# Optimization experiments

Hardware: AMD Instinct MI355X
Metric: run time of the kernel (lower is better)

Reference implementation:

```python
import jax, jax.numpy as jnp
import numpy as np

EMBED_DIM = 1024

def setup_inputs() -> dict:
    key = jax.random.key(0)
    kx, kwq, kbq, kwk, kbk, kwv, kbv = jax.random.split(key, 7)
    d = EMBED_DIM
    s = 1.0 / np.sqrt(d)
    x = jax.random.normal(kx, (4, 2048, d), dtype=jnp.float32)
    # nn.Linear weights are [out, in]; we store transposed [in, out] for x @ W
    Wq = jax.random.uniform(kwq, (d, d), jnp.float32, -s, s)
    bq = jax.random.uniform(kbq, (d,), jnp.float32, -s, s)
    Wk = jax.random.uniform(kwk, (d, d), jnp.float32, -s, s)
    bk = jax.random.uniform(kbk, (d,), jnp.float32, -s, s)
    Wv = jax.random.uniform(kwv, (d, d), jnp.float32, -s, s)
    bv = jax.random.uniform(kbv, (d,), jnp.float32, -s, s)
    return {"x": x, "Wq": Wq, "bq": bq, "Wk": Wk, "bk": bk, "Wv": Wv, "bv": bv}

def reference(x, Wq, bq, Wk, bk, Wv, bv):
    d = x.shape[-1]
    q = x @ Wq + bq            # [B, S, D]
    k = x @ Wk + bk            # [B, S, D]
    v = x @ Wv + bv            # [B, S, D]
    scores = jnp.einsum('bsd,btd->bst', q, k) / jnp.sqrt(jnp.asarray(d, x.dtype))
    attn = jax.nn.softmax(scores, axis=-1)  # [B, S, S]
    return jnp.einsum('bst,btd->bsd', attn, v)
```

## Files before the change

kernel.cpp:

```cpp
#include <hip/hip_runtime.h>
#include <hip/hip_bf16.h>
#include <stdint.h>


typedef short bf16x8 __attribute__((ext_vector_type(8)));
typedef float f32x4 __attribute__((ext_vector_type(4)));
typedef unsigned short us4 __attribute__((ext_vector_type(4)));
typedef unsigned short us8 __attribute__((ext_vector_type(8)));
typedef _Float16 h8v __attribute__((ext_vector_type(8)));
typedef unsigned short us;

#define B_ 4
#define S_ 2048
#define D_ 1024

__device__ __forceinline__ us f2bf(float f) {
  unsigned int u = __float_as_uint(f);
  unsigned int r = (u + 0x7fffu + ((u >> 16) & 1u)) >> 16;
  return (us)r;
}

__device__ __forceinline__ void gl2lds16(void* lds, const void* g) {
  __builtin_amdgcn_global_load_lds(
      (const __attribute__((address_space(1))) unsigned int*)(uintptr_t)g,
      (__attribute__((address_space(3))) unsigned int*)(uintptr_t)lds,
      16, 0, 0);
}

__device__ __forceinline__ void sched_fence() { __builtin_amdgcn_sched_barrier(0); }
__device__ __forceinline__ void barrier_f() {
  sched_fence(); __builtin_amdgcn_s_barrier(); sched_fence();
}

template<int BM, int R0, int R1>
__device__ __forceinline__ void stageR(us* buf, const us* gA, size_t sA,
                                       const us* gB, size_t sB,
                                       int wave, int lane) {
  int slot = ((lane & 7) ^ (lane >> 3)) << 4;
  char* l = (char*)buf;
#pragma unroll
  for (int r = R0; r < R1; ++r) {
    int row = r * 64 + wave * 8 + (lane >> 3);
    const char* src;
    if (r * 64 < BM)
      src = (const char*)gA + (size_t)row * sA + slot;
    else
      src = (const char*)gB + (size_t)(row - BM) * sB + slot;
    gl2lds16(l + r * 8192 + wave * 1024, src);
  }
}

template<int EPI, int BM, int BN, int WNS>
__global__ __launch_bounds__(512, 2) void gemm8p(
    const us* __restrict__ Aall, const us* __restrict__ Ball,
    size_t aBatch, size_t bBatch, int sAe, int sBe, int nt,
    const float* __restrict__ bias1, void* __restrict__ outp,
    us* __restrict__ vtb) {
  __shared__ __align__(16) us lds[3][(BM + BN) * 64];
  int tid = threadIdx.x, lane = tid & 63, wave = tid >> 6;
  int wm = wave / WNS, wn = wave % WNS;
  int m0 = blockIdx.x * BM, n0 = blockIdx.y * BN;
  size_t bz = blockIdx.z;
  const us* gA = Aall + bz * aBatch + (size_t)m0 * sAe;
  const us* gB = Ball + bz * bBatch + (size_t)n0 * sBe;
  size_t sA = (size_t)sAe * 2, sB = (size_t)sBe * 2;

  stageR<BM, 0, 6>(lds[0], gA, sA, gB, sB, wave, lane);
  stageR<BM, 0, 6>(lds[1], gA + 64, sA, gB + 64, sB, wave, lane);

  int r15 = lane & 15, kg = lane >> 4, l7 = lane & 7;
  int x0 = (kg ^ l7) << 4;
  f32x4 acc[4][4] = {};

  for (int t = 0; t < nt; ++t) {
    if (t == nt - 1) asm volatile("s_waitcnt vmcnt(0)" ::: "memory");
    else             asm volatile("s_waitcnt vmcnt(6)" ::: "memory");
    barrier_f();
    const us* buf = lds[t % 3];
    us* nbuf = (us*)lds[(t + 2) % 3];
    bool dostage = (t + 2 < nt);
    const us* gA2 = gA + (size_t)(t + 2) * 64;
    const us* gB2 = gB + (size_t)(t + 2) * 64;
    const char* pa = (const char*)buf + (size_t)(wm * 64 + r15) * 128;
    const char* pb = (const char*)buf + (size_t)(BM + wn * 64 + r15) * 128;

    if (dostage) stageR<BM, 0, 3>(nbuf, gA2, sA, gB2, sB, wave, lane);
    bf16x8 A0[4], B0[4];
#pragma unroll
    for (int f = 0; f < 4; ++f) A0[f] = *(const bf16x8*)(pa + f * 2048 + x0);
#pragma unroll
    for (int f = 0; f < 4; ++f) B0[f] = *(const bf16x8*)(pb + f * 2048 + x0);
    __builtin_amdgcn_s_setprio(1);
#pragma unroll
    for (int fn = 0; fn < 4; ++fn)
#pragma unroll
      for (int fm = 0; fm < 4; ++fm)
        acc[fm][fn] = __builtin_amdgcn_mfma_f32_16x16x32_bf16(A0[fm], B0[fn], acc[fm][fn], 0, 0, 0);
    __builtin_amdgcn_s_setprio(0);

    if (dostage) stageR<BM, 3, 6>(nbuf, gA2, sA, gB2, sB, wave, lane);
    bf16x8 A1[4], B1[4];
#pragma unroll
    for (int f = 0; f < 4; ++f) A1[f] = *(const bf16x8*)(pa + f * 2048 + (x0 ^ 64));
#pragma unroll
    for (int f = 0; f < 4; ++f) B1[f] = *(const bf16x8*)(pb + f * 2048 + (x0 ^ 64));
    __builtin_amdgcn_s_setprio(1);
#pragma unroll
    for (int fn = 0; fn < 4; ++fn)
#pragma unroll
      for (int fm = 0; fm < 4; ++fm)
        acc[fm][fn] = __builtin_amdgcn_mfma_f32_16x16x32_bf16(A1[fm], B1[fn], acc[fm][fn], 0, 0, 0);
    __builtin_amdgcn_s_setprio(0);
  }

#pragma unroll
  for (int fm = 0; fm < 4; ++fm)
#pragma unroll
    for (int fn = 0; fn < 4; ++fn) {
      int col = n0 + wn * 64 + fn * 16 + r15;
      int row0 = m0 + wm * 64 + fm * 16 + ((lane >> 4) << 2);
      if constexpr (EPI == 3) {
        int mat = col >> 10;
        if (mat == 0) {
          us* ob = (us*)outp;
#pragma unroll
          for (int r = 0; r < 4; ++r)
            ob[(size_t)(row0 + r) * D_ + col] = f2bf(acc[fm][fn][r]);
        } else {
          float bb = bias1[col & 1023];
          int b = row0 >> 11, trow = row0 & 2047, dcol = col & 1023;
          us4 v4 = {f2bf(acc[fm][fn][0] + bb), f2bf(acc[fm][fn][1] + bb),
                    f2bf(acc[fm][fn][2] + bb), f2bf(acc[fm][fn][3] + bb)};
          *(us4*)(vtb + (size_t)b * D_ * S_ + (size_t)dcol * S_ + trow) = v4;
        }
      } else {
        float* ob = (float*)outp + bz * (size_t)(S_ * D_);
#pragma unroll
        for (int r = 0; r < 4; ++r)
          ob[(size_t)(row0 + r) * D_ + col] = acc[fm][fn][r];
      }
    }
}

__global__ __launch_bounds__(512, 2) void s2k(
    const us* __restrict__ Aall, const us* __restrict__ Ball,
    const float* __restrict__ cvp, _Float16* __restrict__ scores) {
  __shared__ __align__(16) us lds3[3][16384];
  const int tid = threadIdx.x, lane = tid & 63, wave = tid >> 6;
  const int wm = wave >> 2, wn = wave & 3;
  const int m0 = blockIdx.x * 256, n0 = blockIdx.y * 256;
  const size_t bz = blockIdx.z;
  const char* gA = (const char*)(Aall + bz * (size_t)(S_ * D_) + (size_t)m0 * D_);
  const char* gB = (const char*)(Ball + bz * (size_t)(S_ * D_) + (size_t)n0 * D_);
  const size_t sA = (size_t)D_ * 2, sB = (size_t)D_ * 2;
  const int nt = 32;

  const int r15 = lane & 15, kg = lane >> 4;
  const int srcslot = (((lane & 3) ^ ((lane >> 3) & 3)) << 4);
  const int srow = wave * 16 + (lane >> 2);

  auto stage = [&](int bi, int t) {
    char* l = (char*)lds3[bi];
    const size_t koff = (size_t)t * 64;
#pragma unroll
    for (int r = 0; r < 4; ++r) {
      int row = r * 128 + srow;
      const char* src = (row < 256)
          ? gA + (size_t)row * sA + koff + srcslot
          : gB + (size_t)(row - 256) * sB + koff + srcslot;
      gl2lds16(l + r * 8192 + wave * 1024, src);
    }
  };

  stage(0, 0);
  stage(1, 1);

  f32x4 acc[8][4] = {};
  for (int t = 0; t < nt; ++t) {
    if (t == nt - 1) asm volatile("s_waitcnt vmcnt(0)" ::: "memory");
    else             asm volatile("s_waitcnt vmcnt(4)" ::: "memory");
    barrier_f();
    if (t + 2 < nt) stage((t + 2) % 3, t + 2);
    const char* buf = (const char*)lds3[t % 3];

    bf16x8 Af[8], Bf[4];
#pragma unroll
    for (int f = 0; f < 8; ++f) {
      int tr = wm * 128 + f * 16 + r15;
      Af[f] = *(const bf16x8*)(buf + tr * 64 + ((kg ^ ((tr >> 1) & 3)) << 4));
    }
#pragma unroll
    for (int n = 0; n < 4; ++n) {
      int tr = 256 + wn * 64 + n * 16 + r15;
      Bf[n] = *(const bf16x8*)(buf + tr * 64 + ((kg ^ ((tr >> 1) & 3)) << 4));
    }
    __builtin_amdgcn_s_setprio(1);
#pragma unroll
    for (int n = 0; n < 4; ++n)
#pragma unroll
      for (int f = 0; f < 8; ++f)
        acc[f][n] = __builtin_amdgcn_mfma_f32_16x16x32_bf16(Af[f], Bf[n], acc[f][n], 0, 0, 0);
    __builtin_amdgcn_s_setprio(0);
  }

  _Float16* sc = scores + bz * (size_t)(S_ * S_);
  const float* cb = cvp + bz * (size_t)S_;
#pragma unroll
  for (int fm = 0; fm < 8; ++fm)
#pragma unroll
    for (int fn = 0; fn < 4; ++fn) {
      int col = n0 + wn * 64 + fn * 16 + r15;
      int row0 = m0 + wm * 128 + fm * 16 + ((lane >> 4) << 2);
      float cv = cb[col];
#pragma unroll
      for (int r = 0; r < 4; ++r)
        sc[(size_t)(row0 + r) * S_ + col] = (_Float16)((acc[fm][fn][r] + cv) * 0.03125f);
    }
}

__global__ __launch_bounds__(256) void mprep(const us* __restrict__ wkb,
                                             const us* __restrict__ wqb,
                                             us* __restrict__ mtb) {
  int tid = threadIdx.x, lane = tid & 63, wave = tid >> 6;
  int j0 = blockIdx.x * 64, i0 = blockIdx.y * 64;
  int r15 = lane & 15, kg = lane >> 4;
  f32x4 acc[4] = {};
  for (int kk = 0; kk < D_; kk += 32) {
    bf16x8 a = *(const bf16x8*)(wkb + (size_t)(j0 + wave * 16 + r15) * D_ + kk + kg * 8);
#pragma unroll
    for (int f = 0; f < 4; ++f) {
      bf16x8 b = *(const bf16x8*)(wqb + (size_t)(i0 + f * 16 + r15) * D_ + kk + kg * 8);
      acc[f] = __builtin_amdgcn_mfma_f32_16x16x32_bf16(a, b, acc[f], 0, 0, 0);
    }
  }
#pragma unroll
  for (int f = 0; f < 4; ++f)
#pragma unroll
    for (int r = 0; r < 4; ++r)
      mtb[(size_t)(j0 + wave * 16 + kg * 4 + r) * D_ + i0 + f * 16 + r15] = f2bf(acc[f][r]);
}

__global__ __launch_bounds__(256) void uprep(const float* __restrict__ Wk,
                                             const float* __restrict__ bq,
                                             float* __restrict__ u) {
  int lane = threadIdx.x & 63, wave = threadIdx.x >> 6;
  int i = blockIdx.x * 4 + wave;
  const float* row = Wk + (size_t)i * D_;
  float s = 0.f;
#pragma unroll
  for (int e = 0; e < 4; ++e) {
    float4 a = *(const float4*)(row + e * 256 + lane * 4);
    float4 b = *(const float4*)(bq + e * 256 + lane * 4);
    s += a.x * b.x + a.y * b.y + a.z * b.z + a.w * b.w;
  }
#pragma unroll
  for (int o = 32; o; o >>= 1) s += __shfl_xor(s, o);
  if (lane == 0) u[i] = s;
}

__global__ __launch_bounds__(256) void cvec(const float* __restrict__ x,
                                            const float* __restrict__ u,
                                            float* __restrict__ c) {
  int lane = threadIdx.x & 63, wave = threadIdx.x >> 6;
  int i = blockIdx.x * 4 + wave;
  const float* row = x + (size_t)i * D_;
  float s = 0.f;
#pragma unroll
  for (int e = 0; e < 4; ++e) {
    float4 a = *(const float4*)(row + e * 256 + lane * 4);
    float4 b = *(const float4*)(u + e * 256 + lane * 4);
    s += a.x * b.x + a.y * b.y + a.z * b.z + a.w * b.w;
  }
#pragma unroll
  for (int o = 32; o; o >>= 1) s += __shfl_xor(s, o);
  if (lane == 0) c[i] = s;
}

__global__ __launch_bounds__(256) void wcast(const float* __restrict__ Wq,
                                             const float* __restrict__ Wk,
                                             us* __restrict__ wqb,
                                             us* __restrict__ wkb) {
  size_t i = ((size_t)blockIdx.x * 256 + threadIdx.x) * 8;
  const float* src = blockIdx.y ? Wk : Wq;
  us* dst = blockIdx.y ? wkb : wqb;
  float4 f0 = *(const float4*)(src + i);
  float4 f1 = *(const float4*)(src + i + 4);
  float vals[8] = {f0.x, f0.y, f0.z, f0.w, f1.x, f1.y, f1.z, f1.w};
  union { bf16x8 v; us s_[8]; } H;
#pragma unroll
  for (int e = 0; e < 8; ++e) H.s_[e] = f2bf(vals[e]);
  *(bf16x8*)(dst + i) = H.v;
}

__global__ __launch_bounds__(256) void wtv(const float* __restrict__ W,
                                           us* __restrict__ o) {
  __shared__ us hs[64][65];
  int n0 = blockIdx.x * 64, k0 = blockIdx.y * 64;
  int tid = threadIdx.x;
#pragma unroll
  for (int i = 0; i < 16; ++i) {
    int idx = tid + i * 256;
    int r = idx >> 6, c = idx & 63;
    hs[r][c] = f2bf(W[(size_t)(k0 + r) * D_ + (n0 + c)]);
  }
  __syncthreads();
#pragma unroll
  for (int i = 0; i < 16; ++i) {
    int idx = tid + i * 256;
    int r = idx >> 6, c = idx & 63;
    o[(size_t)(n0 + r) * D_ + (k0 + c)] = hs[c][r];
  }
}

__global__ __launch_bounds__(256) void xcast(const float* __restrict__ x,
                                             us* __restrict__ xb) {
  size_t i = ((size_t)blockIdx.x * 256 + threadIdx.x) * 8;
  float4 f0 = *(const float4*)(x + i);
  float4 f1 = *(const float4*)(x + i + 4);
  float vals[8] = {f0.x, f0.y, f0.z, f0.w, f1.x, f1.y, f1.z, f1.w};
  union { bf16x8 v; us s_[8]; } H;
#pragma unroll
  for (int e = 0; e < 8; ++e) H.s_[e] = f2bf(vals[e]);
  *(bf16x8*)(xb + i) = H.v;
}

__global__ __launch_bounds__(256) void softmax_k(const _Float16* __restrict__ scores,
                                                 us* __restrict__ pb) {
  int row = blockIdx.x, tid = threadIdx.x, lane = tid & 63, wave = tid >> 6;
  const _Float16* s = scores + (size_t)row * S_;
  h8v a8 = *(const h8v*)(s + tid * 8);
  float a[8];
#pragma unroll
  for (int e = 0; e < 8; ++e) a[e] = (float)a8[e];
  float m = a[0];
#pragma unroll
  for (int e = 1; e < 8; ++e) m = fmaxf(m, a[e]);
#pragma unroll
  for (int o = 32; o; o >>= 1) m = fmaxf(m, __shfl_xor(m, o));
  __shared__ float red[4];
  if (lane == 0) red[wave] = m;
  __syncthreads();
  m = fmaxf(fmaxf(red[0], red[1]), fmaxf(red[2], red[3]));
  float p[8];
  float sum = 0.f;
#pragma unroll
  for (int e = 0; e < 8; ++e) { p[e] = expf(a[e] - m); sum += p[e]; }
#pragma unroll
  for (int o = 32; o; o >>= 1) sum += __shfl_xor(sum, o);
  __syncthreads();
  if (lane == 0) red[wave] = sum;
  __syncthreads();
  float inv = 1.0f / (red[0] + red[1] + red[2] + red[3]);
  us8 h;
#pragma unroll
  for (int e = 0; e < 8; ++e) h[e] = f2bf(p[e] * inv);
  *(us8*)(pb + (size_t)row * S_ + tid * 8) = h;
}

extern "C" void kernel_launch(void* const* d_in, const int* in_sizes, int n_in,
                              void* d_out, int out_size, void* d_ws, size_t ws_size,
                              hipStream_t stream) {
  const float* x  = (const float*)d_in[0];
  const float* Wq = (const float*)d_in[1];
  const float* bq = (const float*)d_in[2];
  const float* Wk = (const float*)d_in[3];
  const float* bk = (const float*)d_in[4];
  const float* Wv = (const float*)d_in[5];
  const float* bv = (const float*)d_in[6];
  (void)bk;
  float* out = (float*)d_out;
  char* ws = (char*)d_ws;
  const size_t MB = 1024 * 1024;
  us* eb   = (us*)(ws + 0 * MB);
  us* wqb  = (us*)(ws + 16 * MB);
  us* wkb  = (us*)(ws + 18 * MB);
  float* u = (float*)(ws + 20 * MB);
  float* c = (float*)(ws + 21 * MB);
  us* vtb  = (us*)(ws + 32 * MB);
  us* mtb  = (us*)(ws + 48 * MB);
  us* wvt  = (us*)(ws + 50 * MB);
  us* xb   = (us*)(ws + 54 * MB);
  _Float16* scores = (_Float16*)(ws + 70 * MB);
  us* pb   = (us*)(ws + 102 * MB);

  wcast<<<dim3(512, 2), 256, 0, stream>>>(Wq, Wk, wqb, wkb);
  wtv<<<dim3(16, 16), 256, 0, stream>>>(Wv, wvt);
  xcast<<<dim3(4096), 256, 0, stream>>>(x, xb);
  mprep<<<dim3(16, 16), 256, 0, stream>>>(wkb, wqb, mtb);
  uprep<<<dim3(256), 256, 0, stream>>>(Wk, bq, u);
  cvec<<<dim3(2048), 256, 0, stream>>>(x, u, c);
  gemm8p<3, 128, 256, 4><<<dim3(64, 8, 1), 512, 0, stream>>>(
      xb, mtb, 0, 0, D_, D_, 16, bv, eb, vtb);
  s2k<<<dim3(8, 8, 4), 512, 0, stream>>>(eb, xb, c, scores);
  softmax_k<<<dim3(B_ * S_), 256, 0, stream>>>(scores, pb);
  gemm8p<2, 256, 128, 2><<<dim3(8, 8, 4), 512, 0, stream>>>(
      pb, vtb, (size_t)S_ * S_, (size_t)D_ * S_, S_, S_, 32,
      nullptr, out, nullptr);
}
```

Measured before the change: 167.2 us.

## Unify GEMMs on 256x256 s2k-style kernel and add 256x128 PV kernel

Removes the generic gemm8p kernel and generalizes the s2k 256x256-tile, 8-wave kernel into gemmF, used for both the fused projection GEMM and the scores GEMM. The final attn@V GEMM gets a new s3n kernel with 256x128 tiles on 4 waves, a three-buffer LDS pipeline and a single stage per iteration. Larger tiles are meant to raise data reuse per loaded byte and give each wave more MFMA work per barrier. The cost is more accumulator registers and fewer blocks for the projection GEMM (256 instead of 512), which may lower occupancy or leave CUs underused.

```diff
diff --git a/kernel.cpp b/kernel.cpp
--- a/kernel.cpp
+++ b/kernel.cpp
@@ -32,128 +32,20 @@
   sched_fence(); __builtin_amdgcn_s_barrier(); sched_fence();
 }
 
-template<int BM, int R0, int R1>
-__device__ __forceinline__ void stageR(us* buf, const us* gA, size_t sA,
-                                       const us* gB, size_t sB,
-                                       int wave, int lane) {
-  int slot = ((lane & 7) ^ (lane >> 3)) << 4;
-  char* l = (char*)buf;
-#pragma unroll
-  for (int r = R0; r < R1; ++r) {
-    int row = r * 64 + wave * 8 + (lane >> 3);
-    const char* src;
-    if (r * 64 < BM)
-      src = (const char*)gA + (size_t)row * sA + slot;
-    else
-      src = (const char*)gB + (size_t)(row - BM) * sB + slot;
-    gl2lds16(l + r * 8192 + wave * 1024, src);
-  }
-}
-
-template<int EPI, int BM, int BN, int WNS>
-__global__ __launch_bounds__(512, 2) void gemm8p(
+template<int EPI>
+__global__ __launch_bounds__(512, 2) void gemmF(
     const us* __restrict__ Aall, const us* __restrict__ Ball,
     size_t aBatch, size_t bBatch, int sAe, int sBe, int nt,
-    const float* __restrict__ bias1, void* __restrict__ outp,
+    const float* __restrict__ auxf, void* __restrict__ outp,
     us* __restrict__ vtb) {
-  __shared__ __align__(16) us lds[3][(BM + BN) * 64];
-  int tid = threadIdx.x, lane = tid & 63, wave = tid >> 6;
-  int wm = wave / WNS, wn = wave % WNS;
-  int m0 = blockIdx.x * BM, n0 = blockIdx.y * BN;
-  size_t bz = blockIdx.z;
-  const us* gA = Aall + bz * aBatch + (size_t)m0 * sAe;
-  const us* gB = Ball + bz * bBatch + (size_t)n0 * sBe;
-  size_t sA = (size_t)sAe * 2, sB = (size_t)sBe * 2;
-
-  stageR<BM, 0, 6>(lds[0], gA, sA, gB, sB, wave, lane);
-  stageR<BM, 0, 6>(lds[1], gA + 64, sA, gB + 64, sB, wave, lane);
-
-  int r15 = lane & 15, kg = lane >> 4, l7 = lane & 7;
-  int x0 = (kg ^ l7) << 4;
-  f32x4 acc[4][4] = {};
-
-  for (int t = 0; t < nt; ++t) {
-    if (t == nt - 1) asm volatile("s_waitcnt vmcnt(0)" ::: "memory");
-    else             asm volatile("s_waitcnt vmcnt(6)" ::: "memory");
-    barrier_f();
-    const us* buf = lds[t % 3];
-    us* nbuf = (us*)lds[(t + 2) % 3];
-    bool dostage = (t + 2 < nt);
-    const us* gA2 = gA + (size_t)(t + 2) * 64;
-    const us* gB2 = gB + (size_t)(t + 2) * 64;
-    const char* pa = (const char*)buf + (size_t)(wm * 64 + r15) * 128;
-    const char* pb = (const char*)buf + (size_t)(BM + wn * 64 + r15) * 128;
-
-    if (dostage) stageR<BM, 0, 3>(nbuf, gA2, sA, gB2, sB, wave, lane);
-    bf16x8 A0[4], B0[4];
-#pragma unroll
-    for (int f = 0; f < 4; ++f) A0[f] = *(const bf16x8*)(pa + f * 2048 + x0);
-#pragma unroll
-    for (int f = 0; f < 4; ++f) B0[f] = *(const bf16x8*)(pb + f * 2048 + x0);
-    __builtin_amdgcn_s_setprio(1);
-#pragma unroll
-    for (int fn = 0; fn < 4; ++fn)
-#pragma unroll
-      for (int fm = 0; fm < 4; ++fm)
-        acc[fm][fn] = __builtin_amdgcn_mfma_f32_16x16x32_bf16(A0[fm], B0[fn], acc[fm][fn], 0, 0, 0);
-    __builtin_amdgcn_s_setprio(0);
-
-    if (dostage) stageR<BM, 3, 6>(nbuf, gA2, sA, gB2, sB, wave, lane);
-    bf16x8 A1[4], B1[4];
-#pragma unroll
-    for (int f = 0; f < 4; ++f) A1[f] = *(const bf16x8*)(pa + f * 2048 + (x0 ^ 64));
-#pragma unroll
-    for (int f = 0; f < 4; ++f) B1[f] = *(const bf16x8*)(pb + f * 2048 + (x0 ^ 64));
-    __builtin_amdgcn_s_setprio(1);
-#pragma unroll
-    for (int fn = 0; fn < 4; ++fn)
-#pragma unroll
-      for (int fm = 0; fm < 4; ++fm)
-        acc[fm][fn] = __builtin_amdgcn_mfma_f32_16x16x32_bf16(A1[fm], B1[fn], acc[fm][fn], 0, 0, 0);
-    __builtin_amdgcn_s_setprio(0);
-  }
-
-#pragma unroll
-  for (int fm = 0; fm < 4; ++fm)
-#pragma unroll
-    for (int fn = 0; fn < 4; ++fn) {
-      int col = n0 + wn * 64 + fn * 16 + r15;
-      int row0 = m0 + wm * 64 + fm * 16 + ((lane >> 4) << 2);
-      if constexpr (EPI == 3) {
-        int mat = col >> 10;
-        if (mat == 0) {
-          us* ob = (us*)outp;
-#pragma unroll
-          for (int r = 0; r < 4; ++r)
-            ob[(size_t)(row0 + r) * D_ + col] = f2bf(acc[fm][fn][r]);
-        } else {
-          float bb = bias1[col & 1023];
-          int b = row0 >> 11, trow = row0 & 2047, dcol = col & 1023;
-          us4 v4 = {f2bf(acc[fm][fn][0] + bb), f2bf(acc[fm][fn][1] + bb),
-                    f2bf(acc[fm][fn][2] + bb), f2bf(acc[fm][fn][3] + bb)};
-          *(us4*)(vtb + (size_t)b * D_ * S_ + (size_t)dcol * S_ + trow) = v4;
-        }
-      } else {
-        float* ob = (float*)outp + bz * (size_t)(S_ * D_);
-#pragma unroll
-        for (int r = 0; r < 4; ++r)
-          ob[(size_t)(row0 + r) * D_ + col] = acc[fm][fn][r];
-      }
-    }
-}
-
-__global__ __launch_bounds__(512, 2) void s2k(
-    const us* __restrict__ Aall, const us* __restrict__ Ball,
-    const float* __restrict__ cvp, _Float16* __restrict__ scores) {
   __shared__ __align__(16) us lds3[3][16384];
   const int tid = threadIdx.x, lane = tid & 63, wave = tid >> 6;
   const int wm = wave >> 2, wn = wave & 3;
   const int m0 = blockIdx.x * 256, n0 = blockIdx.y * 256;
   const size_t bz = blockIdx.z;
-  const char* gA = (const char*)(Aall + bz * (size_t)(S_ * D_) + (size_t)m0 * D_);
-  const char* gB = (const char*)(Ball + bz * (size_t)(S_ * D_) + (size_t)n0 * D_);
-  const size_t sA = (size_t)D_ * 2, sB = (size_t)D_ * 2;
-  const int nt = 32;
+  const char* gA = (const char*)(Aall + bz * aBatch) + (size_t)m0 * sAe * 2;
+  const char* gB = (const char*)(Ball + bz * bBatch) + (size_t)n0 * sBe * 2;
+  const size_t sA = (size_t)sAe * 2, sB = (size_t)sBe * 2;
 
   const int r15 = lane & 15, kg = lane >> 4;
   const int srcslot = (((lane & 3) ^ ((lane >> 3) & 3)) << 4);
@@ -203,18 +95,107 @@
     __builtin_amdgcn_s_setprio(0);
   }
 
-  _Float16* sc = scores + bz * (size_t)(S_ * S_);
-  const float* cb = cvp + bz * (size_t)S_;
 #pragma unroll
   for (int fm = 0; fm < 8; ++fm)
 #pragma unroll
     for (int fn = 0; fn < 4; ++fn) {
       int col = n0 + wn * 64 + fn * 16 + r15;
-      int row0 = m0 + wm * 128 + fm * 16 + ((lane >> 4) << 2);
-      float cv = cb[col];
+      int row0 = m0 + wm * 128 + fm * 16 + (kg << 2);
+      if constexpr (EPI == 3) {
+        if ((col >> 10) == 0) {
+          us* ob = (us*)outp;
+#pragma unroll
+          for (int r = 0; r < 4; ++r)
+            ob[(size_t)(row0 + r) * D_ + col] = f2bf(acc[fm][fn][r]);
+        } else {
+          int dcol = col & 1023;
+          float bb = auxf[dcol];
+          int b = row0 >> 11, trow = row0 & 2047;
+          us4 v4 = {f2bf(acc[fm][fn][0] + bb), f2bf(acc[fm][fn][1] + bb),
+                    f2bf(acc[fm][fn][2] + bb), f2bf(acc[fm][fn][3] + bb)};
+          *(us4*)(vtb + (size_t)b * D_ * S_ + (size_t)dcol * S_ + trow) = v4;
+        }
+      } else {
+        _Float16* sc = (_Float16*)outp + bz * (size_t)(S_ * S_);
+        float cv = (auxf + bz * (size_t)S_)[col];
+#pragma unroll
+        for (int r = 0; r < 4; ++r)
+          sc[(size_t)(row0 + r) * S_ + col] = (_Float16)((acc[fm][fn][r] + cv) * 0.03125f);
+      }
+    }
+}
+
+__global__ __launch_bounds__(256, 2) void s3n(
+    const us* __restrict__ pb, const us* __restrict__ vtball,
+    float* __restrict__ outp) {
+  __shared__ __align__(16) us lds3[3][12288];
+  const int tid = threadIdx.x, lane = tid & 63, wave = tid >> 6;
+  const int wm = wave >> 1, wn = wave & 1;
+  const int m0 = blockIdx.x * 256, n0 = blockIdx.y * 128;
+  const size_t bz = blockIdx.z;
+  const char* gA = (const char*)(pb + bz * (size_t)(S_ * S_)) + (size_t)m0 * S_ * 2;
+  const char* gB = (const char*)(vtball + bz * (size_t)(D_ * S_)) + (size_t)n0 * S_ * 2;
+  const size_t sA = (size_t)S_ * 2, sB = (size_t)S_ * 2;
+  const int nt = 64;
+
+  const int r15 = lane & 15, kg = lane >> 4;
+  const int srcslot = (((lane & 3) ^ ((lane >> 3) & 3)) << 4);
+  const int srow = wave * 16 + (lane >> 2);
+
+  auto stage = [&](int bi, int t) {
+    char* l = (char*)lds3[bi];
+    const size_t koff = (size_t)t * 64;
+#pragma unroll
+    for (int r = 0; r < 6; ++r) {
+      int row = r * 64 + srow;
+      const char* src = (row < 256)
+          ? gA + (size_t)row * sA + koff + srcslot
+          : gB + (size_t)(row - 256) * sB + koff + srcslot;
+      gl2lds16(l + r * 4096 + wave * 1024, src);
+    }
+  };
+
+  stage(0, 0);
+  stage(1, 1);
+
+  f32x4 acc[8][4] = {};
+  for (int t = 0; t < nt; ++t) {
+    if (t == nt - 1) asm volatile("s_waitcnt vmcnt(0)" ::: "memory");
+    else             asm volatile("s_waitcnt vmcnt(6)" ::: "memory");
+    barrier_f();
+    if (t + 2 < nt) stage((t + 2) % 3, t + 2);
+    const char* buf = (const char*)lds3[t % 3];
+
+    bf16x8 Af[8], Bf[4];
+#pragma unroll
+    for (int f = 0; f < 8; ++f) {
+      int tr = wm * 128 + f * 16 + r15;
+      Af[f] = *(const bf16x8*)(buf + tr * 64 + ((kg ^ ((tr >> 1) & 3)) << 4));
+    }
+#pragma unroll
+    for (int n = 0; n < 4; ++n) {
+      int tr = 256 + wn * 64 + n * 16 + r15;
+      Bf[n] = *(const bf16x8*)(buf + tr * 64 + ((kg ^ ((tr >> 1) & 3)) << 4));
+    }
+    __builtin_amdgcn_s_setprio(1);
+#pragma unroll
+    for (int n = 0; n < 4; ++n)
+#pragma unroll
+      for (int f = 0; f < 8; ++f)
+        acc[f][n] = __builtin_amdgcn_mfma_f32_16x16x32_bf16(Af[f], Bf[n], acc[f][n], 0, 0, 0);
+    __builtin_amdgcn_s_setprio(0);
+  }
+
+  float* ob = outp + bz * (size_t)(S_ * D_);
+#pragma unroll
+  for (int fm = 0; fm < 8; ++fm)
+#pragma unroll
+    for (int fn = 0; fn < 4; ++fn) {
+      int col = n0 + wn * 64 + fn * 16 + r15;
+      int row0 = m0 + wm * 128 + fm * 16 + (kg << 2);
 #pragma unroll
       for (int r = 0; r < 4; ++r)
-        sc[(size_t)(row0 + r) * S_ + col] = (_Float16)((acc[fm][fn][r] + cv) * 0.03125f);
+        ob[(size_t)(row0 + r) * D_ + col] = acc[fm][fn][r];
     }
 }
 
@@ -382,6 +363,7 @@
   us* xb   = (us*)(ws + 54 * MB);
   _Float16* scores = (_Float16*)(ws + 70 * MB);
   us* pb   = (us*)(ws + 102 * MB);
+  (void)wvt;
 
   wcast<<<dim3(512, 2), 256, 0, stream>>>(Wq, Wk, wqb, wkb);
   wtv<<<dim3(16, 16), 256, 0, stream>>>(Wv, wvt);
@@ -389,11 +371,10 @@
   mprep<<<dim3(16, 16), 256, 0, stream>>>(wkb, wqb, mtb);
   uprep<<<dim3(256), 256, 0, stream>>>(Wk, bq, u);
   cvec<<<dim3(2048), 256, 0, stream>>>(x, u, c);
-  gemm8p<3, 128, 256, 4><<<dim3(64, 8, 1), 512, 0, stream>>>(
-      xb, mtb, 0, 0, D_, D_, 16, bv, eb, vtb);
-  s2k<<<dim3(8, 8, 4), 512, 0, stream>>>(eb, xb, c, scores);
+  gemmF<3><<<dim3(32, 8, 1), 512, 0, stream>>>(
+      xb, mtb, 0, 0, D_, D_, 32, bv, eb, vtb);
+  gemmF<1><<<dim3(8, 8, 4), 512, 0, stream>>>(
+      eb, xb, (size_t)S_ * D_, (size_t)S_ * D_, D_, D_, 32, c, scores, nullptr);
   softmax_k<<<dim3(B_ * S_), 256, 0, stream>>>(scores, pb);
-  gemm8p<2, 256, 128, 2><<<dim3(8, 8, 4), 512, 0, stream>>>(
-      pb, vtb, (size_t)S_ * S_, (size_t)D_ * S_, S_, S_, 32,
-      nullptr, out, nullptr);
-}
+  s3n<<<dim3(8, 8, 4), 256, 0, stream>>>(pb, vtb, out);
+}
```

Measured after the change: 179.1 us. +7.1%, slower.
